# Kernel tuning notes

Measured on AMD Instinct MI355X. Metric: run time of the kernel, lower is better.

Reference implementation:

```python
import jax, jax.numpy as jnp
import numpy as np

NEG_SLOPE = 0.01  # F.leaky_relu default
NUM_GRAPHS = 64


def sage_conv(x, src, dst, W_l, b_l, W_r):
    """PyG SAGEConv (mean aggr): lin_l(mean_j x_j) + lin_r(x_i)."""
    n = x.shape[0]
    msg = x[src]                                               # [E, C] gather
    agg = jax.ops.segment_sum(msg, dst, num_segments=n)        # [N, C] scatter-add
    deg = jax.ops.segment_sum(jnp.ones_like(dst, dtype=x.dtype), dst, num_segments=n)
    mean = agg / jnp.maximum(deg, 1.0)[:, None]
    return mean @ W_l + b_l + x @ W_r


def setup_inputs() -> dict:
    key = jax.random.key(0)
    ks = jax.random.split(key, 12)
    N, E, C, H, O = 50000, 600000, 128, 128, 2
    x = jax.random.normal(ks[0], (N, C), dtype=jnp.float32)
    edge_index = jax.random.randint(ks[1], (2, E), 0, N, dtype=jnp.int64)
    batch = jnp.sort(jax.random.randint(ks[2], (N,), 0, NUM_GRAPHS, dtype=jnp.int64))

    def lin(k, fin, fout):
        return jax.random.normal(k, (fin, fout), dtype=jnp.float32) / np.sqrt(fin)

    return {
        "x": x, "edge_index": edge_index, "batch": batch,
        "W1_l": lin(ks[3], C, H), "b1": jnp.zeros((H,), jnp.float32), "W1_r": lin(ks[4], C, H),
        "W2_l": lin(ks[5], H, H), "b2": jnp.zeros((H,), jnp.float32), "W2_r": lin(ks[6], H, H),
        "W3_l": lin(ks[7], H, H), "b3": jnp.zeros((H,), jnp.float32), "W3_r": lin(ks[8], H, H),
        "W_fc": lin(ks[9], H, O), "b_fc": jnp.zeros((O,), jnp.float32),
    }


def reference(x, edge_index, batch, W1_l, b1, W1_r, W2_l, b2, W2_r,
              W3_l, b3, W3_r, W_fc, b_fc):
    src, dst = edge_index[0], edge_index[1]
    h = jax.nn.leaky_relu(sage_conv(x, src, dst, W1_l, b1, W1_r), NEG_SLOPE)
    h = jax.nn.leaky_relu(sage_conv(h, src, dst, W2_l, b2, W2_r), NEG_SLOPE)
    h = jax.nn.leaky_relu(sage_conv(h, src, dst, W3_l, b3, W3_r), NEG_SLOPE)
    pooled = jax.ops.segment_max(h, batch, num_segments=NUM_GRAPHS)  # global_max_pool
    return pooled @ W_fc + b_fc
```

## Files before the change

kernel.cpp:

```cpp
#include <hip/hip_runtime.h>
#include <hip/hip_bf16.h>

#define NEG_SLOPE 0.01f
#define C 128
#define NGRAPH 64
#define CAP 64

typedef short short8 __attribute__((ext_vector_type(8)));
typedef float f32x4 __attribute__((ext_vector_type(4)));
typedef unsigned short ushort;

__device__ __forceinline__ unsigned fmap(float x){
  unsigned b = __float_as_uint(x);
  return (b & 0x80000000u) ? ~b : (b | 0x80000000u);
}
__device__ __forceinline__ float funmap(unsigned k){
  return (k & 0x80000000u) ? __uint_as_float(k & 0x7FFFFFFFu) : __uint_as_float(~k);
}

__device__ __forceinline__ ushort bf16_rne(float a){
  unsigned u = __float_as_uint(a);
  return (ushort)((u + 0x7FFFu + ((u >> 16) & 1u)) >> 16);
}
__device__ __forceinline__ float b2f(ushort h){
  return __uint_as_float(((unsigned)h) << 16);
}

__device__ __forceinline__ void lds_dma16(const void* g, void* l){
  __builtin_amdgcn_global_load_lds(
      (const __attribute__((address_space(1))) unsigned int*)(void*)g,
      (__attribute__((address_space(3))) unsigned int*)(void*)l, 16, 0, 0);
}

__global__ void prep_kernel(const float* __restrict__ x, ushort* __restrict__ xb, int nx4,
                            const int* __restrict__ src, const int* __restrict__ dst,
                            int* __restrict__ cursor, ushort* __restrict__ csr, int E,
                            const float* __restrict__ W1l, const float* __restrict__ W1r,
                            const float* __restrict__ W2l, const float* __restrict__ W2r,
                            const float* __restrict__ W3l, const float* __restrict__ W3r,
                            short* __restrict__ B1, short* __restrict__ B2,
                            short* __restrict__ B3,
                            int nblk_x, int nblk_e){
  int bid = blockIdx.x;
  if(bid < nblk_e){
    int e = bid * 256 + threadIdx.x;
    if(e < E){
      int d = dst[e];
      int p = atomicAdd(&cursor[d], 1);
      if(p < CAP) csr[(long long)d * CAP + p] = (ushort)src[e];
    }
    return;
  }
  bid -= nblk_e;
  if(bid < nblk_x){
    int i = (bid * 256 + threadIdx.x) * 4;
    if(i < nx4){
      float4 v = *(const float4*)(x + i);
      ushort4 r = make_ushort4(bf16_rne(v.x), bf16_rne(v.y), bf16_rne(v.z), bf16_rne(v.w));
      *(ushort4*)(xb + i) = r;
    }
    return;
  }
  bid -= nblk_x;
  int set = bid >> 7;
  int idx = (bid & 127) * 256 + threadIdx.x;
  const float* Wl = (set == 0) ? W1l : (set == 1) ? W2l : W3l;
  const float* Wr = (set == 0) ? W1r : (set == 1) ? W2r : W3r;
  short* Bpk      = (set == 0) ? B1  : (set == 1) ? B2  : B3;
  int k = idx >> 7, n = idx & 127;
  float w = (k < C) ? Wl[k * C + n] : Wr[(k - C) * C + n];
  ushort hi = bf16_rne(w);
  float r = w - b2f(hi);
  ushort lo = bf16_rne(r);
  int kstep = k >> 5, kg = (k >> 3) & 3, j = k & 7;
  int pos = ((kstep * 4 + kg) * C + n) * 8 + j;
  Bpk[pos] = (short)hi;
  Bpk[pos + 32768] = (short)lo;
}

__global__ __launch_bounds__(256, 2) void layer_fused(
    const ushort* __restrict__ xin, const ushort* __restrict__ csr,
    const int* __restrict__ cnt, const short* __restrict__ Bpk,
    const float* __restrict__ bias,
    ushort* __restrict__ Hout, int M,
    const int* __restrict__ batch, unsigned* __restrict__ pooled)
{
  __shared__ ushort Ms[64 * 136];
  __shared__ __align__(16) ushort Xs[64 * 32];
  int tid = threadIdx.x;
  int bm = blockIdx.x * 64;
  int lane = tid & 63;
  int wn = tid >> 6;
  int lg = lane >> 4;
  int lm = lane & 15;

  {
    int grp = tid >> 4, g15 = tid & 15, gbase = tid & 48;
    float a[4][8];
#pragma unroll
    for(int k = 0; k < 4; k++)
#pragma unroll
      for(int f = 0; f < 8; f++) a[k][f] = 0.f;
    int dg[4];
    const ushort* ep[4];
#pragma unroll
    for(int k = 0; k < 4; k++){
      int node = bm + grp + k * 16;
      if(node < M){
        int d = cnt[node];
        dg[k] = d < CAP ? d : CAP;
        ep[k] = csr + (long long)node * CAP;
      }else{
        dg[k] = 0;
        ep[k] = csr;
      }
    }
    int maxd = dg[0];
    maxd = dg[1] > maxd ? dg[1] : maxd;
    maxd = dg[2] > maxd ? dg[2] : maxd;
    maxd = dg[3] > maxd ? dg[3] : maxd;

    for(int base = 0; base < maxd; base += 16){
      int ids[4];
#pragma unroll
      for(int k = 0; k < 4; k++)
        ids[k] = (base + g15 < dg[k]) ? (int)ep[k][base + g15] : 0;
      int lim = maxd - base; if(lim > 16) lim = 16;
      for(int j = 0; j < lim; j += 4){
        short8 r[4][4];
#pragma unroll
        for(int k = 0; k < 4; k++){
#pragma unroll
          for(int u = 0; u < 4; u++){
            int s = __shfl(ids[k], gbase + j + u, 64);
            r[k][u] = *(const short8*)(xin + (long long)s * C + g15 * 8);
          }
        }
#pragma unroll
        for(int k = 0; k < 4; k++){
#pragma unroll
          for(int u = 0; u < 4; u++){
            if(base + j + u < dg[k]){
#pragma unroll
              for(int f = 0; f < 8; f++) a[k][f] += b2f((ushort)r[k][u][f]);
            }
          }
        }
      }
    }
#pragma unroll
    for(int k = 0; k < 4; k++){
      float sc = 1.0f / fmaxf((float)dg[k], 1.0f);
      short8 o;
#pragma unroll
      for(int f = 0; f < 8; f++) o[f] = (short)bf16_rne(a[k][f] * sc);
      *(short8*)(Ms + (grp + k * 16) * 136 + g15 * 8) = o;
    }
  }

  int srow = tid >> 2;
  int sslice = (tid & 3) ^ ((tid >> 3) & 3);
  int grow = bm + srow; if(grow >= M) grow = M - 1;
  const long long goff = (long long)grow * C + sslice * 8;
  ushort* ldsbase = Xs + wn * 512;

  f32x4 acc[4][2];
#pragma unroll
  for(int i = 0; i < 4; i++)
#pragma unroll
    for(int j = 0; j < 2; j++)
      acc[i][j] = (f32x4){0.f, 0.f, 0.f, 0.f};

  short8 bh[2][2], bl[2][2];
  auto loadB = [&](int ks, int buf){
#pragma unroll
    for(int j = 0; j < 2; j++){
      const short* bp = Bpk + (((ks * 4 + lg) * C) + wn * 32 + j * 16 + lm) * 8;
      bh[buf][j] = *(const short8*)bp;
      bl[buf][j] = *(const short8*)(bp + 32768);
    }
  };
  loadB(0, 0);
  __syncthreads();

#pragma unroll
  for(int ks = 0; ks < 8; ks++){
    if(ks >= 4){
      if(ks > 4) __syncthreads();
      lds_dma16(xin + goff + (ks - 4) * 32, ldsbase);
    }
    if(ks < 7) loadB(ks + 1, (ks + 1) & 1);
    if(ks >= 4) __syncthreads();

    short8 af[4];
    if(ks < 4){
#pragma unroll
      for(int i = 0; i < 4; i++)
        af[i] = *(const short8*)(Ms + (i * 16 + lm) * 136 + ks * 32 + lg * 8);
    }else{
#pragma unroll
      for(int i = 0; i < 4; i++){
        int r = i * 16 + lm;
        int slot = lg ^ ((r >> 1) & 3);
        af[i] = *(const short8*)(Xs + r * 32 + slot * 8);
      }
    }
    int b = ks & 1;
#pragma unroll
    for(int i = 0; i < 4; i++)
#pragma unroll
      for(int j = 0; j < 2; j++){
        acc[i][j] = __builtin_amdgcn_mfma_f32_16x16x32_bf16(af[i], bh[b][j], acc[i][j], 0, 0, 0);
        acc[i][j] = __builtin_amdgcn_mfma_f32_16x16x32_bf16(af[i], bl[b][j], acc[i][j], 0, 0, 0);
      }
  }

  if(pooled == nullptr){
#pragma unroll
    for(int j = 0; j < 2; j++){
      int col = wn * 32 + j * 16 + lm;
      float bv = bias[col];
#pragma unroll
      for(int i = 0; i < 4; i++){
#pragma unroll
        for(int reg = 0; reg < 4; reg++){
          int row = bm + i * 16 + lg * 4 + reg;
          if(row < M){
            float v = acc[i][j][reg] + bv;
            v = v > 0.f ? v : NEG_SLOPE * v;
            Hout[(long long)row * C + col] = bf16_rne(v);
          }
        }
      }
    }
  }else{
#pragma unroll
    for(int i = 0; i < 4; i++){
      int row0 = bm + i * 16 + lg * 4;
      if(row0 >= M) continue;
      bool whole = (row0 + 3 < M);
      int g0 = batch[row0];
      bool same = whole && (batch[row0 + 3] == g0);
#pragma unroll
      for(int j = 0; j < 2; j++){
        int col = wn * 32 + j * 16 + lm;
        float bv = bias[col];
        float v0 = acc[i][j][0] + bv; v0 = v0 > 0.f ? v0 : NEG_SLOPE * v0;
        float v1 = acc[i][j][1] + bv; v1 = v1 > 0.f ? v1 : NEG_SLOPE * v1;
        float v2 = acc[i][j][2] + bv; v2 = v2 > 0.f ? v2 : NEG_SLOPE * v2;
        float v3 = acc[i][j][3] + bv; v3 = v3 > 0.f ? v3 : NEG_SLOPE * v3;
        if(same){
          float m01 = fmaxf(v0, v1), m23 = fmaxf(v2, v3);
          atomicMax(&pooled[g0 * C + col], fmap(fmaxf(m01, m23)));
        }else{
          float vv[4] = {v0, v1, v2, v3};
#pragma unroll
          for(int reg = 0; reg < 4; reg++){
            int row = row0 + reg;
            if(row < M) atomicMax(&pooled[batch[row] * C + col], fmap(vv[reg]));
          }
        }
      }
    }
  }
}

__global__ void fc_kernel(const unsigned* __restrict__ pooled_u, const float* __restrict__ Wfc,
                          const float* __restrict__ bfc, float* __restrict__ out){
  int t = threadIdx.x;
  int g = t >> 1, o = t & 1;
  float s = bfc[o];
  const unsigned* pu = pooled_u + g * C;
#pragma unroll
  for(int k0 = 0; k0 < C; k0 += 4){
    uint4 pv = *(const uint4*)(pu + k0);
    float4 w0 = *(const float4*)(Wfc + k0 * 2);
    float4 w1 = *(const float4*)(Wfc + k0 * 2 + 4);
    float wa = o ? w0.y : w0.x;
    float wb = o ? w0.w : w0.z;
    float wc = o ? w1.y : w1.x;
    float wd = o ? w1.w : w1.z;
    s += funmap(pv.x) * wa + funmap(pv.y) * wb + funmap(pv.z) * wc + funmap(pv.w) * wd;
  }
  out[g * 2 + o] = s;
}

extern "C" void kernel_launch(void* const* d_in, const int* in_sizes, int n_in,
                              void* d_out, int out_size, void* d_ws, size_t ws_size,
                              hipStream_t stream) {
  const float* x    = (const float*)d_in[0];
  const int*   ei   = (const int*)d_in[1];
  const int*   batch= (const int*)d_in[2];
  const float* W1l  = (const float*)d_in[3];
  const float* b1   = (const float*)d_in[4];
  const float* W1r  = (const float*)d_in[5];
  const float* W2l  = (const float*)d_in[6];
  const float* b2   = (const float*)d_in[7];
  const float* W2r  = (const float*)d_in[8];
  const float* W3l  = (const float*)d_in[9];
  const float* b3   = (const float*)d_in[10];
  const float* W3r  = (const float*)d_in[11];
  const float* Wfc  = (const float*)d_in[12];
  const float* bfc  = (const float*)d_in[13];
  float* out = (float*)d_out;

  const int N = in_sizes[0] / C;
  const int E = in_sizes[1] / 2;
  const int* srcv = ei;
  const int* dstv = ei + E;

  char* ws = (char*)d_ws;
  size_t off = 0;
  auto alloc = [&](size_t bytes) -> void* {
    void* p = ws + off;
    off += (bytes + 255) & ~(size_t)255;
    return p;
  };
  int*      cursor = (int*)alloc((size_t)N * 4);
  unsigned* pooled = (unsigned*)alloc((size_t)NGRAPH * C * 4);
  size_t    zbytes = off;
  ushort*   csr    = (ushort*)alloc((size_t)N * CAP * 2);
  ushort*   xb     = (ushort*)alloc((size_t)N * C * 2);
  ushort*   h1b    = (ushort*)alloc((size_t)N * C * 2);
  short*    B1     = (short*)alloc((size_t)2 * 2 * C * C * 2);
  short*    B2     = (short*)alloc((size_t)2 * 2 * C * C * 2);
  short*    B3     = (short*)alloc((size_t)2 * 2 * C * C * 2);

  hipMemsetAsync(cursor, 0, zbytes, stream);

  const int nbe  = (E + 255) / 256;
  const int nbx  = (N * C / 4 + 255) / 256;
  const int nbp  = 3 * 128;
  prep_kernel<<<nbe + nbx + nbp, 256, 0, stream>>>(
      x, xb, N * C, srcv, dstv, cursor, csr, E,
      W1l, W1r, W2l, W2r, W3l, W3r, B1, B2, B3, nbx, nbe);

  int lblocks = (N + 63) / 64;

  layer_fused<<<lblocks, 256, 0, stream>>>(xb, csr, cursor, B1, b1,
                                           h1b, N, nullptr, nullptr);
  layer_fused<<<lblocks, 256, 0, stream>>>(h1b, csr, cursor, B2, b2,
                                           xb, N, nullptr, nullptr);
  layer_fused<<<lblocks, 256, 0, stream>>>(xb, csr, cursor, B3, b3,
                                           nullptr, N, batch, pooled);

  fc_kernel<<<1, 128, 0, stream>>>(pooled, Wfc, bfc, out);
}
```

Measured before the change: 261.1 us.

## Prefetch whole X tile to LDS upfront and pad gather with zero row

The self-feature tile is now fetched into a larger LDS buffer in one async DMA burst before the aggregated-mean MFMA phase. Only one barrier remains, so the loads overlap the first half of the GEMM instead of costing one sync per K-step. Out-of-range neighbor slots in the gather now point to an extra zero row appended to each feature buffer, which removes the per-element degree check in the accumulation loop. In exchange, LDS per block grows from 4 KB to 16 KB for Xs, which could lower occupancy. Padding slots now also perform real gathers of the zero row.

```diff
diff --git a/kernel.cpp b/kernel.cpp
--- a/kernel.cpp
+++ b/kernel.cpp
@@ -34,7 +34,8 @@
 
 __global__ void prep_kernel(const float* __restrict__ x, ushort* __restrict__ xb, int nx4,
                             const int* __restrict__ src, const int* __restrict__ dst,
-                            int* __restrict__ cursor, ushort* __restrict__ csr, int E,
+                            int* __restrict__ cursor, ushort* __restrict__ csr, int E, int N,
+                            ushort* __restrict__ h1b,
                             const float* __restrict__ W1l, const float* __restrict__ W1r,
                             const float* __restrict__ W2l, const float* __restrict__ W2r,
                             const float* __restrict__ W3l, const float* __restrict__ W3r,
@@ -62,20 +63,26 @@
     return;
   }
   bid -= nblk_x;
-  int set = bid >> 7;
-  int idx = (bid & 127) * 256 + threadIdx.x;
-  const float* Wl = (set == 0) ? W1l : (set == 1) ? W2l : W3l;
-  const float* Wr = (set == 0) ? W1r : (set == 1) ? W2r : W3r;
-  short* Bpk      = (set == 0) ? B1  : (set == 1) ? B2  : B3;
-  int k = idx >> 7, n = idx & 127;
-  float w = (k < C) ? Wl[k * C + n] : Wr[(k - C) * C + n];
-  ushort hi = bf16_rne(w);
-  float r = w - b2f(hi);
-  ushort lo = bf16_rne(r);
-  int kstep = k >> 5, kg = (k >> 3) & 3, j = k & 7;
-  int pos = ((kstep * 4 + kg) * C + n) * 8 + j;
-  Bpk[pos] = (short)hi;
-  Bpk[pos + 32768] = (short)lo;
+  if(bid < 384){
+    int set = bid >> 7;
+    int idx = (bid & 127) * 256 + threadIdx.x;
+    const float* Wl = (set == 0) ? W1l : (set == 1) ? W2l : W3l;
+    const float* Wr = (set == 0) ? W1r : (set == 1) ? W2r : W3r;
+    short* Bpk      = (set == 0) ? B1  : (set == 1) ? B2  : B3;
+    int k = idx >> 7, n = idx & 127;
+    float w = (k < C) ? Wl[k * C + n] : Wr[(k - C) * C + n];
+    ushort hi = bf16_rne(w);
+    float r = w - b2f(hi);
+    ushort lo = bf16_rne(r);
+    int kstep = k >> 5, kg = (k >> 3) & 3, j = k & 7;
+    int pos = ((kstep * 4 + kg) * C + n) * 8 + j;
+    Bpk[pos] = (short)hi;
+    Bpk[pos + 32768] = (short)lo;
+    return;
+  }
+  int t = threadIdx.x;
+  if(t < C) xb[(long long)N * C + t] = 0;
+  else      h1b[(long long)N * C + (t - C)] = 0;
 }
 
 __global__ __launch_bounds__(256, 2) void layer_fused(
@@ -86,7 +93,7 @@
     const int* __restrict__ batch, unsigned* __restrict__ pooled)
 {
   __shared__ ushort Ms[64 * 136];
-  __shared__ __align__(16) ushort Xs[64 * 32];
+  __shared__ __align__(16) ushort Xs[4 * 2048];
   int tid = threadIdx.x;
   int bm = blockIdx.x * 64;
   int lane = tid & 63;
@@ -124,7 +131,7 @@
       int ids[4];
 #pragma unroll
       for(int k = 0; k < 4; k++)
-        ids[k] = (base + g15 < dg[k]) ? (int)ep[k][base + g15] : 0;
+        ids[k] = (base + g15 < dg[k]) ? (int)ep[k][base + g15] : M;
       int lim = maxd - base; if(lim > 16) lim = 16;
       for(int j = 0; j < lim; j += 4){
         short8 r[4][4];
@@ -140,10 +147,8 @@
         for(int k = 0; k < 4; k++){
 #pragma unroll
           for(int u = 0; u < 4; u++){
-            if(base + j + u < dg[k]){
-#pragma unroll
-              for(int f = 0; f < 8; f++) a[k][f] += b2f((ushort)r[k][u][f]);
-            }
+#pragma unroll
+            for(int f = 0; f < 8; f++) a[k][f] += b2f((ushort)r[k][u][f]);
           }
         }
       }
@@ -157,12 +162,6 @@
       *(short8*)(Ms + (grp + k * 16) * 136 + g15 * 8) = o;
     }
   }
-
-  int srow = tid >> 2;
-  int sslice = (tid & 3) ^ ((tid >> 3) & 3);
-  int grow = bm + srow; if(grow >= M) grow = M - 1;
-  const long long goff = (long long)grow * C + sslice * 8;
-  ushort* ldsbase = Xs + wn * 512;
 
   f32x4 acc[4][2];
 #pragma unroll
@@ -183,27 +182,47 @@
   loadB(0, 0);
   __syncthreads();
 
-#pragma unroll
-  for(int ks = 0; ks < 8; ks++){
-    if(ks >= 4){
-      if(ks > 4) __syncthreads();
-      lds_dma16(xin + goff + (ks - 4) * 32, ldsbase);
-    }
+  {
+    int rq = lane >> 2, ls = lane & 3;
+#pragma unroll
+    for(int t = 0; t < 4; t++){
+      int u = t * 4 + wn;
+      int s = u >> 2, q = u & 3;
+      int rg = q * 16 + rq;
+      int gs = ls ^ ((rg >> 1) & 3);
+      int grow = bm + rg; if(grow >= M) grow = M - 1;
+      lds_dma16(xin + (long long)grow * C + s * 32 + gs * 8, Xs + u * 512);
+    }
+  }
+
+#pragma unroll
+  for(int ks = 0; ks < 4; ks++){
+    loadB(ks + 1, (ks + 1) & 1);
+    short8 af[4];
+#pragma unroll
+    for(int i = 0; i < 4; i++)
+      af[i] = *(const short8*)(Ms + (i * 16 + lm) * 136 + ks * 32 + lg * 8);
+    int b = ks & 1;
+#pragma unroll
+    for(int i = 0; i < 4; i++)
+#pragma unroll
+      for(int j = 0; j < 2; j++){
+        acc[i][j] = __builtin_amdgcn_mfma_f32_16x16x32_bf16(af[i], bh[b][j], acc[i][j], 0, 0, 0);
+        acc[i][j] = __builtin_amdgcn_mfma_f32_16x16x32_bf16(af[i], bl[b][j], acc[i][j], 0, 0, 0);
+      }
+  }
+
+  __syncthreads();
+
+#pragma unroll
+  for(int ks = 4; ks < 8; ks++){
     if(ks < 7) loadB(ks + 1, (ks + 1) & 1);
-    if(ks >= 4) __syncthreads();
-
     short8 af[4];
-    if(ks < 4){
-#pragma unroll
-      for(int i = 0; i < 4; i++)
-        af[i] = *(const short8*)(Ms + (i * 16 + lm) * 136 + ks * 32 + lg * 8);
-    }else{
-#pragma unroll
-      for(int i = 0; i < 4; i++){
-        int r = i * 16 + lm;
-        int slot = lg ^ ((r >> 1) & 3);
-        af[i] = *(const short8*)(Xs + r * 32 + slot * 8);
-      }
+#pragma unroll
+    for(int i = 0; i < 4; i++){
+      int r = i * 16 + lm;
+      int slot = lg ^ ((r >> 1) & 3);
+      af[i] = *(const short8*)(Xs + (ks - 4) * 2048 + r * 32 + slot * 8);
     }
     int b = ks & 1;
 #pragma unroll
@@ -320,8 +339,8 @@
   unsigned* pooled = (unsigned*)alloc((size_t)NGRAPH * C * 4);
   size_t    zbytes = off;
   ushort*   csr    = (ushort*)alloc((size_t)N * CAP * 2);
-  ushort*   xb     = (ushort*)alloc((size_t)N * C * 2);
-  ushort*   h1b    = (ushort*)alloc((size_t)N * C * 2);
+  ushort*   xb     = (ushort*)alloc((size_t)(N + 1) * C * 2);
+  ushort*   h1b    = (ushort*)alloc((size_t)(N + 1) * C * 2);
   short*    B1     = (short*)alloc((size_t)2 * 2 * C * C * 2);
   short*    B2     = (short*)alloc((size_t)2 * 2 * C * C * 2);
   short*    B3     = (short*)alloc((size_t)2 * 2 * C * C * 2);
@@ -331,8 +350,8 @@
   const int nbe  = (E + 255) / 256;
   const int nbx  = (N * C / 4 + 255) / 256;
   const int nbp  = 3 * 128;
-  prep_kernel<<<nbe + nbx + nbp, 256, 0, stream>>>(
-      x, xb, N * C, srcv, dstv, cursor, csr, E,
+  prep_kernel<<<nbe + nbx + nbp + 1, 256, 0, stream>>>(
+      x, xb, N * C, srcv, dstv, cursor, csr, E, N, h1b,
       W1l, W1r, W2l, W2r, W3l, W3r, B1, B2, B3, nbx, nbe);
 
   int lblocks = (N + 63) / 64;
```

Result: no change. 258.9 us (-0.9%).
